# Kernel tuning notes

Measured on AMD Instinct MI355X. Metric: run time of the kernel, lower is better.

The kernel has to match this reference:

```python
import jax, jax.numpy as jnp
import numpy as np

K = 16          # nsample / knn k
GROUPS = 4      # GroupNorm groups
EPS = 1e-5


def setup_inputs() -> dict:
    key = jax.random.key(0)
    ks = jax.random.split(key, 10)
    B, N = 8, 2048
    x = jax.random.normal(ks[0], (B, 3, N), jnp.float32)
    f = x  # at first call features == coordinates
    w = lambda i, shape: jax.random.normal(ks[i], shape, jnp.float32) * 0.05
    return dict(
        x=x, f=f,
        # input_trans: Conv1d(3 -> 64)
        W_it=w(1, (64, 3)), b_it=jnp.zeros((64,), jnp.float32),
        # layer1: Conv2d(128 -> 128, bias=False) + GroupNorm(4, 128)
        W1=w(2, (128, 128)), gn_g=jnp.ones((128,), jnp.float32), gn_b=jnp.zeros((128,), jnp.float32),
        # mlp1: Conv2d(128->256), Conv2d(256->512)
        Wa=w(3, (256, 128)), ba=jnp.zeros((256,), jnp.float32),
        Wb=w(4, (512, 256)), bb=jnp.zeros((512,), jnp.float32),
        # mlp2: Conv1d(640->256), Conv1d(256->128)
        Wc=w(5, (256, 640)), bc=jnp.zeros((256,), jnp.float32),
        Wd=w(6, (128, 256)), bd=jnp.zeros((128,), jnp.float32),
        # mlp3: Conv1d(128->256), Conv1d(256->512)
        We=w(7, (256, 128)), be=jnp.zeros((256,), jnp.float32),
        Wf=w(8, (512, 256)), bf=jnp.zeros((512,), jnp.float32),
    )


def _knn_idx(x):
    # x: (B, 3, N) -> idx: (B, N, K) indices of K nearest neighbors (self-knn)
    coor = jnp.transpose(x, (0, 2, 1))                       # (B, N, 3)
    sq = jnp.sum(coor * coor, axis=-1)                        # (B, N)
    d = sq[:, :, None] + sq[:, None, :] - 2.0 * jnp.einsum('bnc,bmc->bnm', coor, coor)
    _, idx = jax.lax.top_k(-d, K)                             # smallest distances
    return idx


def _group_norm(y, gamma, beta):
    # y: (B, N, K, C); torch GroupNorm normalizes over (C/g, N, K) per (b, group)
    B, N, Kk, C = y.shape
    yg = y.reshape(B, N, Kk, GROUPS, C // GROUPS)
    mu = jnp.mean(yg, axis=(1, 2, 4), keepdims=True)
    var = jnp.var(yg, axis=(1, 2, 4), keepdims=True)
    yg = (yg - mu) * jax.lax.rsqrt(var + EPS)
    return yg.reshape(B, N, Kk, C) * gamma + beta


def reference(x, f, W_it, b_it, W1, gn_g, gn_b, Wa, ba, Wb, bb, Wc, bc, Wd, bd, We, be, Wf, bf):
    B, _, N = x.shape
    idx = _knn_idx(x)                                          # (B, N, K)

    # input_trans: 1x1 conv over channels, channels-last layout (B, N, C)
    h = jnp.einsum('bcn,oc->bno', f, W_it) + b_it              # (B, N, 64)

    # graph feature: gather neighbors, build [nb - h, h]
    nb = jax.vmap(lambda hb, ib: hb[ib])(h, idx)               # (B, N, K, 64)
    hq = h[:, :, None, :]                                       # (B, N, 1, 64)
    feat = jnp.concatenate([nb - hq, jnp.broadcast_to(hq, nb.shape)], axis=-1)  # (B, N, K, 128)

    # layer1: conv1x1 (no bias) + GroupNorm + LeakyReLU(0.2)
    y = jnp.einsum('bnkc,oc->bnko', feat, W1)                  # (B, N, K, 128)
    y = jax.nn.leaky_relu(_group_norm(y, gn_g, gn_b), 0.2)

    local_base = jnp.max(y, axis=2)                             # (B, N, 128)

    # mlp1 over edges, then max over K and global max over N
    g = jax.nn.relu(jnp.einsum('bnkc,oc->bnko', y, Wa) + ba)    # (B, N, K, 256)
    g = jax.nn.relu(jnp.einsum('bnkc,oc->bnko', g, Wb) + bb)    # (B, N, K, 512)
    gfeat = jnp.max(g, axis=2)                                  # (B, N, 512)
    gmax = jnp.max(gfeat, axis=1, keepdims=True)                # (B, 1, 512)

    cat = jnp.concatenate([local_base, jnp.broadcast_to(gmax, (B, N, 512))], axis=-1)  # (B, N, 640)

    lf = jax.nn.relu(jnp.einsum('bnc,oc->bno', cat, Wc) + bc)   # (B, N, 256)
    lf = jax.nn.relu(jnp.einsum('bnc,oc->bno', lf, Wd) + bd)    # (B, N, 128)

    gl = jax.nn.relu(jnp.einsum('bnc,oc->bno', lf, We) + be)    # (B, N, 256)
    gl = jax.nn.relu(jnp.einsum('bnc,oc->bno', gl, Wf) + bf)    # (B, N, 512)
    gl = jnp.max(gl, axis=1, keepdims=True)                     # (B, 1, 512)

    global_feat = jnp.transpose(gl, (0, 2, 1))                  # (B, 512, 1)
    local_feat = jnp.transpose(lf, (0, 2, 1))                   # (B, 128, N)
    return (global_feat, local_feat)
```

## Files before the change

kernel.cpp:

```cpp
#include <hip/hip_runtime.h>

#define BATCH 8
#define NPTS 2048
#define KNNK 16
#define CH 64
#define CF 128
#define CA 256
#define CB 512
#define CCAT 640
#define CC 256
#define CD 128
#define CE 256
#define CG 512
#define NGRP 4
#define EPSF 1e-5f
#define GF_OFF (BATCH*CG)
#define P 8
#define MROWS (P*KNNK)
#define TM 64

typedef __attribute__((ext_vector_type(8))) short short8v;
typedef __attribute__((ext_vector_type(4))) float f32x4;

__device__ inline short f2bf(float f) {
  union { float f; unsigned u; } v; v.f = f;
  unsigned r = v.u + 0x7fff + ((v.u >> 16) & 1);
  return (short)(r >> 16);
}

#define LIDX(r, c, ROW) ((r)*(ROW) + ((c) ^ (((r)&7)<<3)))

__global__ void k_transpose(const float* __restrict__ src, float* __restrict__ dst,
                            int R, int C) {
  int i = blockIdx.x * 256 + threadIdx.x;
  if (i < R * C) {
    int r = i / C, c = i - r * C;
    dst[c * R + r] = src[i];
  }
}

__global__ void k_pack(const float* __restrict__ W, short* __restrict__ Wp,
                       int O, int C, int ld) {
  int tid = blockIdx.x * 256 + threadIdx.x;
  int KS = C >> 5;
  int total = (O >> 4) * KS * 64;
  if (tid >= total) return;
  int l = tid & 63;
  int fs = tid >> 6;
  int nt = fs / KS, ks = fs - nt * KS;
  int o = nt * 16 + (l & 15);
  int c = ks * 32 + (l >> 4) * 8;
  const float* src = W + (size_t)o * ld + c;
  short8v v;
#pragma unroll
  for (int j = 0; j < 8; ++j) v[j] = f2bf(src[j]);
  *(short8v*)&Wp[(size_t)tid * 8] = v;
}

__global__ void k_sq_h(const float* __restrict__ x, const float* __restrict__ f,
                       const float* __restrict__ Wit, const float* __restrict__ bit,
                       float* __restrict__ h) {
  int t = blockIdx.x * 256 + threadIdx.x;
  if (t >= BATCH * NPTS * CH) return;
  int o = t & (CH - 1);
  int bn = t >> 6;
  int n = bn & (NPTS - 1);
  int b = bn >> 11;
  float f0 = f[(b*3 + 0)*NPTS + n];
  float f1 = f[(b*3 + 1)*NPTS + n];
  float f2 = f[(b*3 + 2)*NPTS + n];
  h[t] = f0*Wit[o*3+0] + f1*Wit[o*3+1] + f2*Wit[o*3+2] + bit[o];
}

__global__ __launch_bounds__(256)
void k_knn(const float* __restrict__ x, int* __restrict__ idxout) {
  __shared__ float xs0[2112], xs1[2112], xs2[2112], sqs[2112];
  int blk = blockIdx.x;
  int b = blk >> 9;
  int n0 = (blk & 511) * 4;
  int t = threadIdx.x;
  for (int i = t; i < NPTS; i += 256) {
    float x0 = x[(b*3 + 0)*NPTS + i];
    float x1 = x[(b*3 + 1)*NPTS + i];
    float x2 = x[(b*3 + 2)*NPTS + i];
    int a = (i >> 5)*33 + (i & 31);
    xs0[a] = x0; xs1[a] = x1; xs2[a] = x2;
    sqs[a] = __fadd_rn(__fadd_rn(__fmul_rn(x0,x0), __fmul_rn(x1,x1)), __fmul_rn(x2,x2));
  }
  __syncthreads();
  int lane = t & 63, wv = t >> 6;
  int q = n0 + wv;
  int qa = (q >> 5)*33 + (q & 31);
  float qx = xs0[qa], qy = xs1[qa], qz = xs2[qa];
  float sqq = sqs[qa];
  float d[32];
  int base = lane * 32;
#pragma unroll
  for (int jj = 0; jj < 32; ++jj) {
    int a = lane*33 + jj;
    float mx = xs0[a], my = xs1[a], mz = xs2[a];
    float dot = __fadd_rn(__fadd_rn(__fmul_rn(qx,mx), __fmul_rn(qy,my)), __fmul_rn(qz,mz));
    d[jj] = __fsub_rn(__fadd_rn(sqq, sqs[a]), __fadd_rn(dot, dot));
  }
  const float FINF = __builtin_inff();
  float sv0 = d[0]; int si0 = base;
#pragma unroll
  for (int jj = 1; jj < 16; ++jj)
    if (d[jj] < sv0) { sv0 = d[jj]; si0 = base + jj; }
  float sv1 = d[16]; int si1 = base + 16;
#pragma unroll
  for (int jj = 17; jj < 32; ++jj)
    if (d[jj] < sv1) { sv1 = d[jj]; si1 = base + jj; }
  int gsel = 0;
#pragma unroll
  for (int r = 0; r < KNNK; ++r) {
    float v = sv0; int i = si0;
    if (sv1 < v || (sv1 == v && si1 < i)) { v = sv1; i = si1; }
#pragma unroll
    for (int off = 32; off > 0; off >>= 1) {
      float v2 = __shfl_xor(v, off);
      int   i2 = __shfl_xor(i, off);
      if (v2 < v || (v2 == v && i2 < i)) { v = v2; i = i2; }
    }
    if (lane == r) gsel = i;
    int rem = ((i >> 5) == lane) ? (i & 31) : 64;
    if (rem < 16) {
      float nv = FINF; int ni = 0x7fffffff;
#pragma unroll
      for (int jj = 0; jj < 16; ++jj) {
        float dv = (jj == rem) ? FINF : d[jj];
        d[jj] = dv;
        if (dv < nv) { nv = dv; ni = base + jj; }
      }
      sv0 = nv; si0 = ni;
    } else if (rem < 32) {
      float nv = FINF; int ni = 0x7fffffff;
#pragma unroll
      for (int jj = 16; jj < 32; ++jj) {
        float dv = (jj == rem) ? FINF : d[jj];
        d[jj] = dv;
        if (dv < nv) { nv = dv; ni = base + jj; }
      }
      sv1 = nv; si1 = ni;
    }
  }
  if (lane < KNNK) idxout[(size_t)(b*NPTS + q)*KNNK + lane] = gsel;
}

__device__ inline void stage_feat(short* featS, const float* __restrict__ h,
                                  const int* __restrict__ idx, int b, int n0, int t) {
  int r = t >> 1, cb = (t & 1) * 32;
  int p = r >> 4, kk = r & 15;
  int nbi = idx[(size_t)(b*NPTS + n0 + p)*KNNK + kk];
  const float* hq = h + (size_t)(b*NPTS + n0 + p)*CH;
  const float* hn = h + (size_t)(b*NPTS + nbi)*CH;
#pragma unroll
  for (int j = 0; j < 32; j += 8) {
    float4 q0 = *(const float4*)(hq + cb + j);
    float4 q1 = *(const float4*)(hq + cb + j + 4);
    float4 a0 = *(const float4*)(hn + cb + j);
    float4 a1 = *(const float4*)(hn + cb + j + 4);
    short8v dv, qv;
    dv[0]=f2bf(a0.x-q0.x); dv[1]=f2bf(a0.y-q0.y); dv[2]=f2bf(a0.z-q0.z); dv[3]=f2bf(a0.w-q0.w);
    dv[4]=f2bf(a1.x-q1.x); dv[5]=f2bf(a1.y-q1.y); dv[6]=f2bf(a1.z-q1.z); dv[7]=f2bf(a1.w-q1.w);
    qv[0]=f2bf(q0.x); qv[1]=f2bf(q0.y); qv[2]=f2bf(q0.z); qv[3]=f2bf(q0.w);
    qv[4]=f2bf(q1.x); qv[5]=f2bf(q1.y); qv[6]=f2bf(q1.z); qv[7]=f2bf(q1.w);
    *(short8v*)&featS[LIDX(r, cb + j, CF)] = dv;
    *(short8v*)&featS[LIDX(r, 64 + cb + j, CF)] = qv;
  }
}

__global__ __launch_bounds__(256, 2)
void k_stats(const float* __restrict__ h, const int* __restrict__ idx,
             const short* __restrict__ W1p, float* __restrict__ partials) {
  __shared__ short featS[MROWS*CF];
  int blk = blockIdx.x;
  int b = blk >> 8;
  int n0 = (blk & 255) * P;
  int t = threadIdx.x;
  stage_feat(featS, h, idx, b, n0, t);
  __syncthreads();
  int lane = t & 63, wv = t >> 6;
  int r16 = lane & 15, g8 = (lane >> 4) * 8;
  short8v af[8][4];
#pragma unroll
  for (int m = 0; m < 8; ++m)
#pragma unroll
    for (int ks = 0; ks < 4; ++ks)
      af[m][ks] = *(const short8v*)&featS[LIDX(m*16 + r16, ks*32 + g8, CF)];
  float s = 0.f, ss = 0.f;
#pragma unroll
  for (int n = 0; n < 2; ++n) {
    int nt = 2*wv + n;
    short8v bfr[4];
#pragma unroll
    for (int ks = 0; ks < 4; ++ks)
      bfr[ks] = *(const short8v*)&W1p[(size_t)((nt*4 + ks)*64 + lane)*8];
#pragma unroll
    for (int m = 0; m < 8; ++m) {
      f32x4 acc = {0.f, 0.f, 0.f, 0.f};
#pragma unroll
      for (int ks = 0; ks < 4; ++ks)
        acc = __builtin_amdgcn_mfma_f32_16x16x32_bf16(af[m][ks], bfr[ks], acc, 0, 0, 0);
#pragma unroll
      for (int i = 0; i < 4; ++i) { s += acc[i]; ss += acc[i]*acc[i]; }
    }
  }
#pragma unroll
  for (int off = 32; off > 0; off >>= 1) {
    s += __shfl_xor(s, off);
    ss += __shfl_xor(ss, off);
  }
  if (lane == 0) {
    partials[(size_t)(blk*NGRP + wv)*2 + 0] = s;
    partials[(size_t)(blk*NGRP + wv)*2 + 1] = ss;
  }
}

__global__ void k_reduce(const float* __restrict__ partials, float* __restrict__ stats) {
  int b = blockIdx.x >> 2, g = blockIdx.x & 3;
  int t = threadIdx.x;
  float s  = partials[(size_t)((b*256 + t)*NGRP + g)*2 + 0];
  float ss = partials[(size_t)((b*256 + t)*NGRP + g)*2 + 1];
  __shared__ float rs[256], rss[256];
  rs[t] = s; rss[t] = ss;
  __syncthreads();
  for (int st = 128; st > 0; st >>= 1) {
    if (t < st) { rs[t] += rs[t+st]; rss[t] += rss[t+st]; }
    __syncthreads();
  }
  if (t == 0) {
    const float cnt = (float)((size_t)NPTS * KNNK * 32);
    float mu = rs[0] / cnt;
    float var = rss[0] / cnt - mu*mu;
    stats[(b*NGRP+g)*2+0] = mu;
    stats[(b*NGRP+g)*2+1] = rsqrtf(var + EPSF);
  }
}

__global__ __launch_bounds__(256, 2)
void k_main(const float* __restrict__ h, const int* __restrict__ idx,
            const short* __restrict__ W1p, const float* __restrict__ gng,
            const float* __restrict__ gnb, const float* __restrict__ stats,
            const short* __restrict__ Wap, const float* __restrict__ ba,
            const short* __restrict__ Wbp, const float* __restrict__ bb,
            float* __restrict__ lbase, unsigned* __restrict__ gmaxU) {
  __shared__ short lds[MROWS*CA];
  short* featS = lds;
  short* ynS   = lds + MROWS*CF;
  short* g1S   = lds;
  int blk = blockIdx.x;
  int b = blk >> 8;
  int n0 = (blk & 255) * P;
  int t = threadIdx.x;
  stage_feat(featS, h, idx, b, n0, t);
  __syncthreads();
  int lane = t & 63, wv = t >> 6;
  int r16 = lane & 15, g8 = (lane >> 4) * 8;
  int rowg = (lane >> 4) * 4;
  {
    short8v af[8][4];
#pragma unroll
    for (int m = 0; m < 8; ++m)
#pragma unroll
      for (int ks = 0; ks < 4; ++ks)
        af[m][ks] = *(const short8v*)&featS[LIDX(m*16 + r16, ks*32 + g8, CF)];
    float mu  = stats[(b*NGRP + wv)*2 + 0];
    float rsg = stats[(b*NGRP + wv)*2 + 1];
#pragma unroll
    for (int n = 0; n < 2; ++n) {
      int nt = 2*wv + n;
      int o = nt*16 + r16;
      short8v bfr[4];
#pragma unroll
      for (int ks = 0; ks < 4; ++ks)
        bfr[ks] = *(const short8v*)&W1p[(size_t)((nt*4 + ks)*64 + lane)*8];
      float ga = gng[o], bev = gnb[o];
#pragma unroll
      for (int m = 0; m < 8; ++m) {
        f32x4 acc = {0.f, 0.f, 0.f, 0.f};
#pragma unroll
        for (int ks = 0; ks < 4; ++ks)
          acc = __builtin_amdgcn_mfma_f32_16x16x32_bf16(af[m][ks], bfr[ks], acc, 0, 0, 0);
        float vmax = -3.0e38f;
#pragma unroll
        for (int i = 0; i < 4; ++i) {
          float v = (acc[i] - mu) * rsg * ga + bev;
          v = (v >= 0.f) ? v : 0.2f*v;
          vmax = fmaxf(vmax, v);
          ynS[LIDX(m*16 + rowg + i, o, CF)] = f2bf(v);
        }
        vmax = fmaxf(vmax, __shfl_xor(vmax, 16));
        vmax = fmaxf(vmax, __shfl_xor(vmax, 32));
        if (lane < 16) lbase[(size_t)(b*NPTS + n0 + m)*CF + o] = vmax;
      }
    }
  }
  __syncthreads();
  {
    short8v yf[8][4];
#pragma unroll
    for (int m = 0; m < 8; ++m)
#pragma unroll
      for (int ks = 0; ks < 4; ++ks)
        yf[m][ks] = *(const short8v*)&ynS[LIDX(m*16 + r16, ks*32 + g8, CF)];
    __syncthreads();
#pragma unroll
    for (int nn = 0; nn < 4; ++nn) {
      int nt = wv*4 + nn;
      int o = nt*16 + r16;
      short8v bfr[4];
#pragma unroll
      for (int ks = 0; ks < 4; ++ks)
        bfr[ks] = *(const short8v*)&Wap[(size_t)((nt*4 + ks)*64 + lane)*8];
      float bav = ba[o];
#pragma unroll
      for (int m = 0; m < 8; ++m) {
        f32x4 acc = {0.f, 0.f, 0.f, 0.f};
#pragma unroll
        for (int ks = 0; ks < 4; ++ks)
          acc = __builtin_amdgcn_mfma_f32_16x16x32_bf16(yf[m][ks], bfr[ks], acc, 0, 0, 0);
#pragma unroll
        for (int i = 0; i < 4; ++i) {
          float v = fmaxf(acc[i] + bav, 0.f);
          g1S[LIDX(m*16 + rowg + i, o, CA)] = f2bf(v);
        }
      }
    }
  }
  __syncthreads();
#pragma unroll
  for (int half = 0; half < 2; ++half) {
    f32x4 acc[4][8];
#pragma unroll
    for (int nn = 0; nn < 4; ++nn)
#pragma unroll
      for (int m = 0; m < 8; ++m) acc[nn][m] = (f32x4){0.f, 0.f, 0.f, 0.f};
#pragma unroll
    for (int ks = 0; ks < 8; ++ks) {
      short8v gfk[8];
#pragma unroll
      for (int m = 0; m < 8; ++m)
        gfk[m] = *(const short8v*)&g1S[LIDX(m*16 + r16, ks*32 + g8, CA)];
#pragma unroll
      for (int nn = 0; nn < 4; ++nn) {
        int nt = wv*8 + half*4 + nn;
        short8v bfr = *(const short8v*)&Wbp[(size_t)((nt*8 + ks)*64 + lane)*8];
#pragma unroll
        for (int m = 0; m < 8; ++m)
          acc[nn][m] = __builtin_amdgcn_mfma_f32_16x16x32_bf16(gfk[m], bfr, acc[nn][m], 0, 0, 0);
      }
    }
#pragma unroll
    for (int nn = 0; nn < 4; ++nn) {
      int nt = wv*8 + half*4 + nn;
      float b0 = bb[nt*16 + r16];
      float am = 0.f;
#pragma unroll
      for (int m = 0; m < 8; ++m)
#pragma unroll
        for (int i = 0; i < 4; ++i) am = fmaxf(am, acc[nn][m][i] + b0);
      am = fmaxf(am, __shfl_xor(am, 16));
      am = fmaxf(am, __shfl_xor(am, 32));
      if (lane < 16) atomicMax(&gmaxU[b*CG + nt*16 + lane], __float_as_uint(am));
    }
  }
}

__global__ void k_gbias(const unsigned* __restrict__ gmaxU, const float* __restrict__ WcT,
                        const float* __restrict__ bc, float* __restrict__ bceff) {
  int b = blockIdx.x;
  int o = threadIdx.x;
  float acc = bc[o];
  for (int c = 0; c < CB; ++c)
    acc += __uint_as_float(gmaxU[b*CG + c]) * WcT[(size_t)(CF + c)*CC + o];
  bceff[b*CC + o] = acc;
}

__global__ __launch_bounds__(256)
void k_tail(const float* __restrict__ lbase, const float* __restrict__ bceff,
            const short* __restrict__ WcLp,
            const short* __restrict__ Wdp, const float* __restrict__ bd,
            const short* __restrict__ Wep, const float* __restrict__ be,
            const short* __restrict__ Wfp, const float* __restrict__ bf,
            float* __restrict__ out, unsigned* __restrict__ glmaxU) {
  __shared__ short aS0[TM*CF];
  __shared__ short aS1[TM*CA];
  int blk = blockIdx.x;
  int b = blk >> 5;
  int n0 = (blk & 31) * TM;
  int t = threadIdx.x;
  {
    int r = t >> 2, cb = (t & 3) * 32;
    const float* src = lbase + (size_t)(b*NPTS + n0 + r)*CF + cb;
#pragma unroll
    for (int j = 0; j < 32; j += 8) {
      float4 v0 = *(const float4*)(src + j);
      float4 v1 = *(const float4*)(src + j + 4);
      short8v pv;
      pv[0]=f2bf(v0.x); pv[1]=f2bf(v0.y); pv[2]=f2bf(v0.z); pv[3]=f2bf(v0.w);
      pv[4]=f2bf(v1.x); pv[5]=f2bf(v1.y); pv[6]=f2bf(v1.z); pv[7]=f2bf(v1.w);
      *(short8v*)&aS0[LIDX(r, cb + j, CF)] = pv;
    }
  }
  __syncthreads();
  int lane = t & 63, wv = t >> 6;
  int r16 = lane & 15, g8 = (lane >> 4) * 8;
  int rowg = (lane >> 4) * 4;
  {
    short8v af[4][4];
#pragma unroll
    for (int mt = 0; mt < 4; ++mt)
#pragma unroll
      for (int ks = 0; ks < 4; ++ks)
        af[mt][ks] = *(const short8v*)&aS0[LIDX(mt*16 + r16, ks*32 + g8, CF)];
#pragma unroll
    for (int nn = 0; nn < 4; ++nn) {
      int nt = wv*4 + nn;
      int o = nt*16 + r16;
      short8v bfr[4];
#pragma unroll
      for (int ks = 0; ks < 4; ++ks)
        bfr[ks] = *(const short8v*)&WcLp[(size_t)((nt*4 + ks)*64 + lane)*8];
      float bce = bceff[b*CC + o];
#pragma unroll
      for (int mt = 0; mt < 4; ++mt) {
        f32x4 acc = {0.f, 0.f, 0.f, 0.f};
#pragma unroll
        for (int ks = 0; ks < 4; ++ks)
          acc = __builtin_amdgcn_mfma_f32_16x16x32_bf16(af[mt][ks], bfr[ks], acc, 0, 0, 0);
#pragma unroll
        for (int i = 0; i < 4; ++i)
          aS1[LIDX(mt*16 + rowg + i, o, CA)] = f2bf(fmaxf(acc[i] + bce, 0.f));
      }
    }
  }
  __syncthreads();
  {
    short8v af[4][8];
#pragma unroll
    for (int mt = 0; mt < 4; ++mt)
#pragma unroll
      for (int ks = 0; ks < 8; ++ks)
        af[mt][ks] = *(const short8v*)&aS1[LIDX(mt*16 + r16, ks*32 + g8, CA)];
#pragma unroll
    for (int nn = 0; nn < 2; ++nn) {
      int nt = wv*2 + nn;
      int o = nt*16 + r16;
      short8v bfr[8];
#pragma unroll
      for (int ks = 0; ks < 8; ++ks)
        bfr[ks] = *(const short8v*)&Wdp[(size_t)((nt*8 + ks)*64 + lane)*8];
      float bdv = bd[o];
#pragma unroll
      for (int mt = 0; mt < 4; ++mt) {
        f32x4 acc = {0.f, 0.f, 0.f, 0.f};
#pragma unroll
        for (int ks = 0; ks < 8; ++ks)
          acc = __builtin_amdgcn_mfma_f32_16x16x32_bf16(af[mt][ks], bfr[ks], acc, 0, 0, 0);
#pragma unroll
        for (int i = 0; i < 4; ++i) {
          float v = fmaxf(acc[i] + bdv, 0.f);
          aS0[LIDX(mt*16 + rowg + i, o, CF)] = f2bf(v);
          out[GF_OFF + ((size_t)(b*CD + o))*NPTS + n0 + mt*16 + rowg + i] = v;
        }
      }
    }
  }
  __syncthreads();
  {
    short8v af[4][4];
#pragma unroll
    for (int mt = 0; mt < 4; ++mt)
#pragma unroll
      for (int ks = 0; ks < 4; ++ks)
        af[mt][ks] = *(const short8v*)&aS0[LIDX(mt*16 + r16, ks*32 + g8, CF)];
#pragma unroll
    for (int nn = 0; nn < 4; ++nn) {
      int nt = wv*4 + nn;
      int o = nt*16 + r16;
      short8v bfr[4];
#pragma unroll
      for (int ks = 0; ks < 4; ++ks)
        bfr[ks] = *(const short8v*)&Wep[(size_t)((nt*4 + ks)*64 + lane)*8];
      float bev = be[o];
#pragma unroll
      for (int mt = 0; mt < 4; ++mt) {
        f32x4 acc = {0.f, 0.f, 0.f, 0.f};
#pragma unroll
        for (int ks = 0; ks < 4; ++ks)
          acc = __builtin_amdgcn_mfma_f32_16x16x32_bf16(af[mt][ks], bfr[ks], acc, 0, 0, 0);
#pragma unroll
        for (int i = 0; i < 4; ++i)
          aS1[LIDX(mt*16 + rowg + i, o, CA)] = f2bf(fmaxf(acc[i] + bev, 0.f));
      }
    }
  }
  __syncthreads();
  {
    short8v af[4][8];
#pragma unroll
    for (int mt = 0; mt < 4; ++mt)
#pragma unroll
      for (int ks = 0; ks < 8; ++ks)
        af[mt][ks] = *(const short8v*)&aS1[LIDX(mt*16 + r16, ks*32 + g8, CA)];
#pragma unroll
    for (int nn = 0; nn < 8; ++nn) {
      int nt = wv*8 + nn;
      short8v bfr[8];
#pragma unroll
      for (int ks = 0; ks < 8; ++ks)
        bfr[ks] = *(const short8v*)&Wfp[(size_t)((nt*8 + ks)*64 + lane)*8];
      float bfv = bf[nt*16 + r16];
      float am = 0.f;
#pragma unroll
      for (int mt = 0; mt < 4; ++mt) {
        f32x4 acc = {0.f, 0.f, 0.f, 0.f};
#pragma unroll
        for (int ks = 0; ks < 8; ++ks)
          acc = __builtin_amdgcn_mfma_f32_16x16x32_bf16(af[mt][ks], bfr[ks], acc, 0, 0, 0);
#pragma unroll
        for (int i = 0; i < 4; ++i) am = fmaxf(am, acc[i] + bfv);
      }
      am = fmaxf(am, __shfl_xor(am, 16));
      am = fmaxf(am, __shfl_xor(am, 32));
      if (lane < 16) atomicMax(&glmaxU[b*CG + nt*16 + lane], __float_as_uint(am));
    }
  }
}

__global__ void k_final(const unsigned* __restrict__ glmaxU, float* __restrict__ out) {
  int i = blockIdx.x*256 + threadIdx.x;
  if (i < BATCH*CG) out[i] = __uint_as_float(glmaxU[i]);
}

extern "C" void kernel_launch(void* const* d_in, const int* in_sizes, int n_in,
                              void* d_out, int out_size, void* d_ws, size_t ws_size,
                              hipStream_t stream) {
  const float* x   = (const float*)d_in[0];
  const float* f   = (const float*)d_in[1];
  const float* Wit = (const float*)d_in[2];
  const float* bit = (const float*)d_in[3];
  const float* W1  = (const float*)d_in[4];
  const float* gng = (const float*)d_in[5];
  const float* gnb = (const float*)d_in[6];
  const float* Wa  = (const float*)d_in[7];
  const float* ba  = (const float*)d_in[8];
  const float* Wb  = (const float*)d_in[9];
  const float* bb  = (const float*)d_in[10];
  const float* Wc  = (const float*)d_in[11];
  const float* bc  = (const float*)d_in[12];
  const float* Wd  = (const float*)d_in[13];
  const float* bd  = (const float*)d_in[14];
  const float* We  = (const float*)d_in[15];
  const float* be  = (const float*)d_in[16];
  const float* Wf  = (const float*)d_in[17];
  const float* bf  = (const float*)d_in[18];
  float* out = (float*)d_out;

  char* w = (char*)d_ws;
  size_t off = 0;
  auto alloc = [&](size_t bytes) {
    void* p = w + off; off += (bytes + 255) & ~(size_t)255; return p;
  };
  float* h        = (float*)alloc((size_t)BATCH*NPTS*CH*4);
  int*   idx      = (int*)  alloc((size_t)BATCH*NPTS*KNNK*4);
  short* W1p      = (short*)alloc((size_t)CF*CF*2);
  short* Wap      = (short*)alloc((size_t)CA*CF*2);
  short* Wbp      = (short*)alloc((size_t)CB*CA*2);
  short* WcLp     = (short*)alloc((size_t)CC*CF*2);
  short* Wdp      = (short*)alloc((size_t)CD*CC*2);
  short* Wep      = (short*)alloc((size_t)CE*CD*2);
  short* Wfp      = (short*)alloc((size_t)CG*CE*2);
  float* WcT      = (float*)alloc((size_t)CCAT*CC*4);
  float* bceff    = (float*)alloc((size_t)BATCH*CC*4);
  float* partials = (float*)alloc((size_t)(BATCH*NPTS/P)*NGRP*2*4);
  float* stats    = (float*)alloc((size_t)BATCH*NGRP*2*4);
  float* lbase    = (float*)alloc((size_t)BATCH*NPTS*CF*4);
  unsigned* gmaxU  = (unsigned*)alloc((size_t)BATCH*CG*4);
  unsigned* glmaxU = (unsigned*)alloc((size_t)BATCH*CG*4);

  hipMemsetAsync(gmaxU, 0, (size_t)BATCH*CG*4, stream);
  hipMemsetAsync(glmaxU, 0, (size_t)BATCH*CG*4, stream);

  k_pack<<<8,  256, 0, stream>>>(W1, W1p, CF, CF, CF);
  k_pack<<<16, 256, 0, stream>>>(Wa, Wap, CA, CF, CF);
  k_pack<<<64, 256, 0, stream>>>(Wb, Wbp, CB, CA, CA);
  k_pack<<<16, 256, 0, stream>>>(Wc, WcLp, CC, CF, CCAT);
  k_pack<<<16, 256, 0, stream>>>(Wd, Wdp, CD, CC, CC);
  k_pack<<<16, 256, 0, stream>>>(We, Wep, CE, CD, CD);
  k_pack<<<64, 256, 0, stream>>>(Wf, Wfp, CG, CE, CE);
  k_transpose<<<(CC*CCAT+255)/256, 256, 0, stream>>>(Wc, WcT, CC, CCAT);

  k_sq_h<<<(BATCH*NPTS*CH+255)/256, 256, 0, stream>>>(x, f, Wit, bit, h);
  k_knn<<<BATCH*NPTS/4, 256, 0, stream>>>(x, idx);
  k_stats<<<BATCH*NPTS/P, 256, 0, stream>>>(h, idx, W1p, partials);
  k_reduce<<<BATCH*NGRP, 256, 0, stream>>>(partials, stats);
  k_main<<<BATCH*NPTS/P, 256, 0, stream>>>(h, idx, W1p, gng, gnb, stats,
                                           Wap, ba, Wbp, bb, lbase, gmaxU);
  k_gbias<<<BATCH, 256, 0, stream>>>(gmaxU, WcT, bc, bceff);
  k_tail<<<BATCH*NPTS/TM, 256, 0, stream>>>(lbase, bceff, WcLp, Wdp, bd,
                                            Wep, be, Wfp, bf, out, glmaxU);
  k_final<<<(BATCH*CG+255)/256, 256, 0, stream>>>(glmaxU, out);
}
```

Measured before the change: 300.8 us.

## Shrink k_main tile to four points, merge prep kernels, rewrite gbias reduction

The main edge-MLP kernel now handles 4 points (64 rows) per block instead of 8. This halves LDS and accumulator register use and allows 4 blocks per CU, for better occupancy and twice as many blocks. Feature staging is re-split so each thread handles either the difference half or the centre half. The weight packing and input-transform kernels are merged into one launch. The Wc transpose is dropped in favour of a wave-reduced gbias kernel that reads Wc rows directly. The trade-off is less reuse of each weight fragment per block, so more weight traffic from L2.

```diff
diff --git a/kernel.cpp b/kernel.cpp
--- a/kernel.cpp
+++ b/kernel.cpp
@@ -15,8 +15,10 @@
 #define NGRP 4
 #define EPSF 1e-5f
 #define GF_OFF (BATCH*CG)
-#define P 8
-#define MROWS (P*KNNK)
+#define PS 8
+#define MRS (PS*KNNK)
+#define PM 4
+#define MRM (PM*KNNK)
 #define TM 64
 
 typedef __attribute__((ext_vector_type(8))) short short8v;
@@ -30,18 +32,8 @@
 
 #define LIDX(r, c, ROW) ((r)*(ROW) + ((c) ^ (((r)&7)<<3)))
 
-__global__ void k_transpose(const float* __restrict__ src, float* __restrict__ dst,
-                            int R, int C) {
-  int i = blockIdx.x * 256 + threadIdx.x;
-  if (i < R * C) {
-    int r = i / C, c = i - r * C;
-    dst[c * R + r] = src[i];
-  }
-}
-
-__global__ void k_pack(const float* __restrict__ W, short* __restrict__ Wp,
-                       int O, int C, int ld) {
-  int tid = blockIdx.x * 256 + threadIdx.x;
+__device__ inline void pack_dev(const float* __restrict__ W, short* __restrict__ Wp,
+                                int O, int C, int ld, int tid) {
   int KS = C >> 5;
   int total = (O >> 4) * KS * 64;
   if (tid >= total) return;
@@ -57,19 +49,34 @@
   *(short8v*)&Wp[(size_t)tid * 8] = v;
 }
 
-__global__ void k_sq_h(const float* __restrict__ x, const float* __restrict__ f,
-                       const float* __restrict__ Wit, const float* __restrict__ bit,
-                       float* __restrict__ h) {
-  int t = blockIdx.x * 256 + threadIdx.x;
-  if (t >= BATCH * NPTS * CH) return;
-  int o = t & (CH - 1);
-  int bn = t >> 6;
-  int n = bn & (NPTS - 1);
-  int b = bn >> 11;
-  float f0 = f[(b*3 + 0)*NPTS + n];
-  float f1 = f[(b*3 + 1)*NPTS + n];
-  float f2 = f[(b*3 + 2)*NPTS + n];
-  h[t] = f0*Wit[o*3+0] + f1*Wit[o*3+1] + f2*Wit[o*3+2] + bit[o];
+__global__ __launch_bounds__(256)
+void k_prep(const float* __restrict__ f, const float* __restrict__ Wit,
+            const float* __restrict__ bit, float* __restrict__ h,
+            const float* __restrict__ W1, short* __restrict__ W1p,
+            const float* __restrict__ Wa, short* __restrict__ Wap,
+            const float* __restrict__ Wb, short* __restrict__ Wbp,
+            const float* __restrict__ Wc, short* __restrict__ WcLp,
+            const float* __restrict__ Wd, short* __restrict__ Wdp,
+            const float* __restrict__ We, short* __restrict__ Wep,
+            const float* __restrict__ Wf, short* __restrict__ Wfp) {
+  int blk = blockIdx.x;
+  if (blk < 4096) {
+    int t = blk * 256 + threadIdx.x;
+    int o = t & (CH - 1);
+    int bn = t >> 6;
+    int n = bn & (NPTS - 1);
+    int b = bn >> 11;
+    float f0 = f[(b*3 + 0)*NPTS + n];
+    float f1 = f[(b*3 + 1)*NPTS + n];
+    float f2 = f[(b*3 + 2)*NPTS + n];
+    h[t] = f0*Wit[o*3+0] + f1*Wit[o*3+1] + f2*Wit[o*3+2] + bit[o];
+  } else if (blk < 4104) pack_dev(W1, W1p, CF, CF, CF, (blk-4096)*256 + threadIdx.x);
+  else if (blk < 4120) pack_dev(Wa, Wap, CA, CF, CF, (blk-4104)*256 + threadIdx.x);
+  else if (blk < 4184) pack_dev(Wb, Wbp, CB, CA, CA, (blk-4120)*256 + threadIdx.x);
+  else if (blk < 4200) pack_dev(Wc, WcLp, CC, CF, CCAT, (blk-4184)*256 + threadIdx.x);
+  else if (blk < 4216) pack_dev(Wd, Wdp, CD, CC, CC, (blk-4200)*256 + threadIdx.x);
+  else if (blk < 4232) pack_dev(We, Wep, CE, CD, CD, (blk-4216)*256 + threadIdx.x);
+  else                 pack_dev(Wf, Wfp, CG, CE, CE, (blk-4232)*256 + threadIdx.x);
 }
 
 __global__ __launch_bounds__(256)
@@ -147,8 +154,8 @@
   if (lane < KNNK) idxout[(size_t)(b*NPTS + q)*KNNK + lane] = gsel;
 }
 
-__device__ inline void stage_feat(short* featS, const float* __restrict__ h,
-                                  const int* __restrict__ idx, int b, int n0, int t) {
+__device__ inline void stage_feat8(short* featS, const float* __restrict__ h,
+                                   const int* __restrict__ idx, int b, int n0, int t) {
   int r = t >> 1, cb = (t & 1) * 32;
   int p = r >> 4, kk = r & 15;
   int nbi = idx[(size_t)(b*NPTS + n0 + p)*KNNK + kk];
@@ -173,12 +180,12 @@
 __global__ __launch_bounds__(256, 2)
 void k_stats(const float* __restrict__ h, const int* __restrict__ idx,
              const short* __restrict__ W1p, float* __restrict__ partials) {
-  __shared__ short featS[MROWS*CF];
+  __shared__ short featS[MRS*CF];
   int blk = blockIdx.x;
   int b = blk >> 8;
-  int n0 = (blk & 255) * P;
+  int n0 = (blk & 255) * PS;
   int t = threadIdx.x;
-  stage_feat(featS, h, idx, b, n0, t);
+  stage_feat8(featS, h, idx, b, n0, t);
   __syncthreads();
   int lane = t & 63, wv = t >> 6;
   int r16 = lane & 15, g8 = (lane >> 4) * 8;
@@ -238,30 +245,60 @@
   }
 }
 
-__global__ __launch_bounds__(256, 2)
+__global__ __launch_bounds__(256, 4)
 void k_main(const float* __restrict__ h, const int* __restrict__ idx,
             const short* __restrict__ W1p, const float* __restrict__ gng,
             const float* __restrict__ gnb, const float* __restrict__ stats,
             const short* __restrict__ Wap, const float* __restrict__ ba,
             const short* __restrict__ Wbp, const float* __restrict__ bb,
             float* __restrict__ lbase, unsigned* __restrict__ gmaxU) {
-  __shared__ short lds[MROWS*CA];
+  __shared__ short lds[MRM*CA];
   short* featS = lds;
-  short* ynS   = lds + MROWS*CF;
+  short* ynS   = lds + MRM*CF;
   short* g1S   = lds;
   int blk = blockIdx.x;
-  int b = blk >> 8;
-  int n0 = (blk & 255) * P;
+  int b = blk >> 9;
+  int n0 = (blk & 511) * PM;
   int t = threadIdx.x;
-  stage_feat(featS, h, idx, b, n0, t);
+  {
+    int r = t >> 2, q4 = (t & 3) * 32;
+    int p = r >> 4, kk = r & 15;
+    const float* hq = h + (size_t)(b*NPTS + n0 + p)*CH;
+    if (q4 < 64) {
+      int nbi = idx[(size_t)(b*NPTS + n0 + p)*KNNK + kk];
+      const float* hn = h + (size_t)(b*NPTS + nbi)*CH;
+#pragma unroll
+      for (int j = 0; j < 32; j += 8) {
+        float4 q0 = *(const float4*)(hq + q4 + j);
+        float4 q1 = *(const float4*)(hq + q4 + j + 4);
+        float4 a0 = *(const float4*)(hn + q4 + j);
+        float4 a1 = *(const float4*)(hn + q4 + j + 4);
+        short8v dv;
+        dv[0]=f2bf(a0.x-q0.x); dv[1]=f2bf(a0.y-q0.y); dv[2]=f2bf(a0.z-q0.z); dv[3]=f2bf(a0.w-q0.w);
+        dv[4]=f2bf(a1.x-q1.x); dv[5]=f2bf(a1.y-q1.y); dv[6]=f2bf(a1.z-q1.z); dv[7]=f2bf(a1.w-q1.w);
+        *(short8v*)&featS[LIDX(r, q4 + j, CF)] = dv;
+      }
+    } else {
+      int cb = q4 - 64;
+#pragma unroll
+      for (int j = 0; j < 32; j += 8) {
+        float4 q0 = *(const float4*)(hq + cb + j);
+        float4 q1 = *(const float4*)(hq + cb + j + 4);
+        short8v qv;
+        qv[0]=f2bf(q0.x); qv[1]=f2bf(q0.y); qv[2]=f2bf(q0.z); qv[3]=f2bf(q0.w);
+        qv[4]=f2bf(q1.x); qv[5]=f2bf(q1.y); qv[6]=f2bf(q1.z); qv[7]=f2bf(q1.w);
+        *(short8v*)&featS[LIDX(r, q4 + j, CF)] = qv;
+      }
+    }
+  }
   __syncthreads();
   int lane = t & 63, wv = t >> 6;
   int r16 = lane & 15, g8 = (lane >> 4) * 8;
   int rowg = (lane >> 4) * 4;
   {
-    short8v af[8][4];
-#pragma unroll
-    for (int m = 0; m < 8; ++m)
+    short8v af[4][4];
+#pragma unroll
+    for (int m = 0; m < 4; ++m)
 #pragma unroll
       for (int ks = 0; ks < 4; ++ks)
         af[m][ks] = *(const short8v*)&featS[LIDX(m*16 + r16, ks*32 + g8, CF)];
@@ -277,7 +314,7 @@
         bfr[ks] = *(const short8v*)&W1p[(size_t)((nt*4 + ks)*64 + lane)*8];
       float ga = gng[o], bev = gnb[o];
 #pragma unroll
-      for (int m = 0; m < 8; ++m) {
+      for (int m = 0; m < 4; ++m) {
         f32x4 acc = {0.f, 0.f, 0.f, 0.f};
 #pragma unroll
         for (int ks = 0; ks < 4; ++ks)
@@ -298,9 +335,9 @@
   }
   __syncthreads();
   {
-    short8v yf[8][4];
-#pragma unroll
-    for (int m = 0; m < 8; ++m)
+    short8v yf[4][4];
+#pragma unroll
+    for (int m = 0; m < 4; ++m)
 #pragma unroll
       for (int ks = 0; ks < 4; ++ks)
         yf[m][ks] = *(const short8v*)&ynS[LIDX(m*16 + r16, ks*32 + g8, CF)];
@@ -315,7 +352,7 @@
         bfr[ks] = *(const short8v*)&Wap[(size_t)((nt*4 + ks)*64 + lane)*8];
       float bav = ba[o];
 #pragma unroll
-      for (int m = 0; m < 8; ++m) {
+      for (int m = 0; m < 4; ++m) {
         f32x4 acc = {0.f, 0.f, 0.f, 0.f};
 #pragma unroll
         for (int ks = 0; ks < 4; ++ks)
@@ -331,23 +368,23 @@
   __syncthreads();
 #pragma unroll
   for (int half = 0; half < 2; ++half) {
-    f32x4 acc[4][8];
+    f32x4 acc[4][4];
 #pragma unroll
     for (int nn = 0; nn < 4; ++nn)
 #pragma unroll
-      for (int m = 0; m < 8; ++m) acc[nn][m] = (f32x4){0.f, 0.f, 0.f, 0.f};
+      for (int m = 0; m < 4; ++m) acc[nn][m] = (f32x4){0.f, 0.f, 0.f, 0.f};
 #pragma unroll
     for (int ks = 0; ks < 8; ++ks) {
-      short8v gfk[8];
-#pragma unroll
-      for (int m = 0; m < 8; ++m)
+      short8v gfk[4];
+#pragma unroll
+      for (int m = 0; m < 4; ++m)
         gfk[m] = *(const short8v*)&g1S[LIDX(m*16 + r16, ks*32 + g8, CA)];
 #pragma unroll
       for (int nn = 0; nn < 4; ++nn) {
         int nt = wv*8 + half*4 + nn;
         short8v bfr = *(const short8v*)&Wbp[(size_t)((nt*8 + ks)*64 + lane)*8];
 #pragma unroll
-        for (int m = 0; m < 8; ++m)
+        for (int m = 0; m < 4; ++m)
           acc[nn][m] = __builtin_amdgcn_mfma_f32_16x16x32_bf16(gfk[m], bfr, acc[nn][m], 0, 0, 0);
       }
     }
@@ -357,7 +394,7 @@
       float b0 = bb[nt*16 + r16];
       float am = 0.f;
 #pragma unroll
-      for (int m = 0; m < 8; ++m)
+      for (int m = 0; m < 4; ++m)
 #pragma unroll
         for (int i = 0; i < 4; ++i) am = fmaxf(am, acc[nn][m][i] + b0);
       am = fmaxf(am, __shfl_xor(am, 16));
@@ -367,14 +404,22 @@
   }
 }
 
-__global__ void k_gbias(const unsigned* __restrict__ gmaxU, const float* __restrict__ WcT,
-                        const float* __restrict__ bc, float* __restrict__ bceff) {
+__global__ __launch_bounds__(256)
+void k_gbias(const unsigned* __restrict__ gmaxU, const float* __restrict__ Wc,
+             const float* __restrict__ bc, float* __restrict__ bceff) {
+  __shared__ float gs[CB];
   int b = blockIdx.x;
-  int o = threadIdx.x;
-  float acc = bc[o];
-  for (int c = 0; c < CB; ++c)
-    acc += __uint_as_float(gmaxU[b*CG + c]) * WcT[(size_t)(CF + c)*CC + o];
-  bceff[b*CC + o] = acc;
+  int t = threadIdx.x;
+  int lane = t & 63, wv = t >> 6;
+  for (int i = t; i < CB; i += 256) gs[i] = __uint_as_float(gmaxU[b*CG + i]);
+  __syncthreads();
+  for (int o = wv; o < CC; o += 4) {
+    float acc = 0.f;
+    for (int c = lane; c < CB; c += 64) acc += gs[c] * Wc[(size_t)o*CCAT + CF + c];
+#pragma unroll
+    for (int off = 32; off > 0; off >>= 1) acc += __shfl_xor(acc, off);
+    if (lane == 0) bceff[b*CC + o] = bc[o] + acc;
+  }
 }
 
 __global__ __launch_bounds__(256)
@@ -572,9 +617,8 @@
   short* Wdp      = (short*)alloc((size_t)CD*CC*2);
   short* Wep      = (short*)alloc((size_t)CE*CD*2);
   short* Wfp      = (short*)alloc((size_t)CG*CE*2);
-  float* WcT      = (float*)alloc((size_t)CCAT*CC*4);
   float* bceff    = (float*)alloc((size_t)BATCH*CC*4);
-  float* partials = (float*)alloc((size_t)(BATCH*NPTS/P)*NGRP*2*4);
+  float* partials = (float*)alloc((size_t)(BATCH*NPTS/PS)*NGRP*2*4);
   float* stats    = (float*)alloc((size_t)BATCH*NGRP*2*4);
   float* lbase    = (float*)alloc((size_t)BATCH*NPTS*CF*4);
   unsigned* gmaxU  = (unsigned*)alloc((size_t)BATCH*CG*4);
@@ -583,22 +627,14 @@
   hipMemsetAsync(gmaxU, 0, (size_t)BATCH*CG*4, stream);
   hipMemsetAsync(glmaxU, 0, (size_t)BATCH*CG*4, stream);
 
-  k_pack<<<8,  256, 0, stream>>>(W1, W1p, CF, CF, CF);
-  k_pack<<<16, 256, 0, stream>>>(Wa, Wap, CA, CF, CF);
-  k_pack<<<64, 256, 0, stream>>>(Wb, Wbp, CB, CA, CA);
-  k_pack<<<16, 256, 0, stream>>>(Wc, WcLp, CC, CF, CCAT);
-  k_pack<<<16, 256, 0, stream>>>(Wd, Wdp, CD, CC, CC);
-  k_pack<<<16, 256, 0, stream>>>(We, Wep, CE, CD, CD);
-  k_pack<<<64, 256, 0, stream>>>(Wf, Wfp, CG, CE, CE);
-  k_transpose<<<(CC*CCAT+255)/256, 256, 0, stream>>>(Wc, WcT, CC, CCAT);
-
-  k_sq_h<<<(BATCH*NPTS*CH+255)/256, 256, 0, stream>>>(x, f, Wit, bit, h);
+  k_prep<<<4296, 256, 0, stream>>>(f, Wit, bit, h, W1, W1p, Wa, Wap, Wb, Wbp,
+                                   Wc, WcLp, Wd, Wdp, We, Wep, Wf, Wfp);
   k_knn<<<BATCH*NPTS/4, 256, 0, stream>>>(x, idx);
-  k_stats<<<BATCH*NPTS/P, 256, 0, stream>>>(h, idx, W1p, partials);
+  k_stats<<<BATCH*NPTS/PS, 256, 0, stream>>>(h, idx, W1p, partials);
   k_reduce<<<BATCH*NGRP, 256, 0, stream>>>(partials, stats);
-  k_main<<<BATCH*NPTS/P, 256, 0, stream>>>(h, idx, W1p, gng, gnb, stats,
-                                           Wap, ba, Wbp, bb, lbase, gmaxU);
-  k_gbias<<<BATCH, 256, 0, stream>>>(gmaxU, WcT, bc, bceff);
+  k_main<<<BATCH*NPTS/PM, 256, 0, stream>>>(h, idx, W1p, gng, gnb, stats,
+                                            Wap, ba, Wbp, bb, lbase, gmaxU);
+  k_gbias<<<BATCH, 256, 0, stream>>>(gmaxU, Wc, bc, bceff);
   k_tail<<<BATCH*NPTS/TM, 256, 0, stream>>>(lbase, bceff, WcLp, Wdp, bd,
                                             Wep, be, Wfp, bf, out, glmaxU);
   k_final<<<(BATCH*CG+255)/256, 256, 0, stream>>>(glmaxU, out);
```

Result: slower. 377.2 us (+25.4%).
